# Optimization experiments

Measured on AMD Instinct MI355X. Metric: run time of the kernel, lower is better.

Reference implementation:

```python
import jax, jax.numpy as jnp
import numpy as np

C = 36   # num_classes
H = 256  # hidden_dim


def setup_inputs() -> dict:
    key = jax.random.key(0)
    ks = jax.random.split(key, 12)
    B, L, Dl, Dg = 32, 196, 1024, 1024
    s = lambda d: 1.0 / np.sqrt(d)
    return {
        "local_features": jax.random.normal(ks[0], (B, L, Dl), jnp.float32),
        "global_average_pool": jax.random.normal(ks[1], (B, Dg), jnp.float32),
        "Wl": jax.random.normal(ks[2], (Dl, C * H), jnp.float32) * s(Dl),
        "bl": jax.random.normal(ks[3], (C * H,), jnp.float32) * s(Dl),
        "Wg": jax.random.normal(ks[4], (Dg, C * H), jnp.float32) * s(Dg),
        "bg": jax.random.normal(ks[5], (C * H,), jnp.float32) * s(Dg),
        "Wh": jax.random.normal(ks[6], (H, H), jnp.float32) * s(H),
        "bh": jax.random.normal(ks[7], (H,), jnp.float32) * s(H),
        "Wr": jax.random.normal(ks[8], (H, 4), jnp.float32) * s(H),
        "br": jax.random.normal(ks[9], (4,), jnp.float32) * s(H),
        "Wc": jax.random.normal(ks[10], (H, 1), jnp.float32) * s(H),
        "bc": jax.random.normal(ks[11], (1,), jnp.float32) * s(H),
    }


def reference(local_features, global_average_pool, Wl, bl, Wg, bg, Wh, bh, Wr, br, Wc, bc):
    B, L, _ = local_features.shape
    # global projection -> [B, C, H]
    xg = (global_average_pool @ Wg + bg).reshape(B, C, H)
    # local projection -> [B, L, C, H] -> [B, C, L, H]
    xl = (local_features @ Wl + bl).reshape(B, L, C, H).transpose(0, 2, 1, 3)
    # per-class attention scores over locations: [B, C, L]
    dot = jnp.einsum('bch,bclh->bcl', xg, xl)
    attn = jax.nn.softmax(dot, axis=-1)
    # attention-weighted sum over locations: [B, C, H]
    ws = jnp.einsum('bcl,bclh->bch', attn, xl)
    hid = jax.nn.relu(ws @ Wh + bh)
    bbox_coords = (hid @ Wr + br).reshape(B, C * 4)   # [B, 4C]
    bbox_presence = (hid @ Wc + bc)[..., 0]           # [B, C]
    return bbox_coords, bbox_presence
```

## Files before the change

kernel.cpp:

```cpp
#include <hip/hip_runtime.h>
#include <stdint.h>

#define NCLS 36
#define HDIM 256
#define BSZ  32
#define LLOC 196
#define DIN  1024
#define NCH  9216
#define NCH4 2304
#define XG_N 294912
#define SC_N 225792
#define SC_N4 56448
#define V_N  1179648

__device__ __forceinline__ void fma4(float4& a, float s, const float4& b) {
  a.x += s * b.x; a.y += s * b.y; a.z += s * b.z; a.w += s * b.w;
}
__device__ __forceinline__ float dot4(const float4& a, const float4& b) {
  return a.x * b.x + a.y * b.y + a.z * b.z + a.w * b.w;
}

__global__ __launch_bounds__(256) void kA_xg(
    const float* __restrict__ Wg, const float* __restrict__ gap,
    float* __restrict__ XGP) {
  __shared__ __align__(16) float4 gs[1024];
  const int tid = threadIdx.x;
  const int nt = blockIdx.x, ks = blockIdx.y;
  const int n0 = nt * 128, k0 = ks * 128;
  const float4* gap4 = (const float4*)gap;
  for (int i = tid; i < 1024; i += 256)
    gs[i] = gap4[(size_t)(i >> 5) * 256 + ks * 32 + (i & 31)];
  __syncthreads();
  const int ng = tid & 31, b0 = (tid >> 5) * 4;
  float4 acc[4] = {};
  const float* wp = Wg + (size_t)k0 * NCH + n0 + ng * 4;
  #pragma unroll 4
  for (int k4 = 0; k4 < 32; ++k4) {
    float4 w[4];
    #pragma unroll
    for (int kk = 0; kk < 4; ++kk)
      w[kk] = *(const float4*)(wp + (size_t)(k4 * 4 + kk) * NCH);
    #pragma unroll
    for (int bb = 0; bb < 4; ++bb) {
      float4 g = gs[(b0 + bb) * 32 + k4];
      fma4(acc[bb], g.x, w[0]); fma4(acc[bb], g.y, w[1]);
      fma4(acc[bb], g.z, w[2]); fma4(acc[bb], g.w, w[3]);
    }
  }
  #pragma unroll
  for (int bb = 0; bb < 4; ++bb)
    *(float4*)&XGP[(size_t)ks * XG_N + (size_t)(b0 + bb) * NCH + n0 + ng * 4] = acc[bb];
}

__global__ __launch_bounds__(256) void kB_red(
    const float* __restrict__ XGP, const float* __restrict__ bg,
    float* __restrict__ XG) {
  const int b = blockIdx.x / 9;
  const int j = (blockIdx.x % 9) * 256 + threadIdx.x;
  const size_t off = (size_t)b * NCH4 + j;
  const float4* p4 = (const float4*)XGP;
  float4 s = ((const float4*)bg)[j];
  #pragma unroll
  for (int p = 0; p < 8; ++p) {
    float4 t = p4[(size_t)p * (XG_N / 4) + off];
    s.x += t.x; s.y += t.y; s.z += t.z; s.w += t.w;
  }
  ((float4*)XG)[off] = s;
}

__global__ __launch_bounds__(128) void kC_V(
    const float* __restrict__ Wl, const float* __restrict__ XG,
    float* __restrict__ V) {
  __shared__ __align__(16) float4 xs[2048];
  const int tid = threadIdx.x;
  const int c = blockIdx.x, kt = blockIdx.y;
  const int k0 = kt * 32;
  const float4* xg4 = (const float4*)XG;
  for (int i = tid; i < 2048; i += 128) {
    int b = i >> 6, h4 = i & 63;
    xs[i] = xg4[(size_t)b * NCH4 + c * 64 + h4];
  }
  __syncthreads();
  const int lane = tid & 63, wv_ = tid >> 6;
  const int q = lane & 3, r = lane >> 2;
  const int b0 = wv_ * 16;
  const int krow = k0 + r * 2;
  float acc0[16] = {}; float acc1[16] = {};
  const float* wl = Wl + (size_t)krow * NCH + c * 256 + q * 4;
  #pragma unroll 4
  for (int it = 0; it < 16; ++it) {
    float4 w0 = *(const float4*)(wl + it * 16);
    float4 w1 = *(const float4*)(wl + NCH + it * 16);
    #pragma unroll
    for (int bb = 0; bb < 16; ++bb) {
      float4 x = xs[(b0 + bb) * 64 + it * 4 + q];
      acc0[bb] += dot4(w0, x);
      acc1[bb] += dot4(w1, x);
    }
  }
  #pragma unroll
  for (int bb = 0; bb < 16; ++bb) {
    float s0 = acc0[bb], s1 = acc1[bb];
    s0 += __shfl_xor(s0, 1); s0 += __shfl_xor(s0, 2);
    s1 += __shfl_xor(s1, 1); s1 += __shfl_xor(s1, 2);
    acc0[bb] = s0; acc1[bb] = s1;
  }
  if (q == 0) {
    #pragma unroll
    for (int bb = 0; bb < 16; ++bb) {
      size_t o = (size_t)((b0 + bb) * NCLS + c) * DIN + krow;
      V[o]     = acc0[bb];
      V[o + 1] = acc1[bb];
    }
  }
}

__global__ __launch_bounds__(256) void kD_scores(
    const float* __restrict__ local_f, const float* __restrict__ V,
    float* __restrict__ SCP) {
  __shared__ __align__(16) float4 loc_s[3136];
  __shared__ __align__(16) float4 v_s[576];
  const int tid = threadIdx.x;
  const int b = blockIdx.x, ks = blockIdx.y;
  const float4* lf4 = (const float4*)local_f;
  for (int i = tid; i < 3136; i += 256) {
    int r = i >> 4, g = i & 15;
    loc_s[r * 16 + ((g + r) & 15)] = lf4[(size_t)(b * LLOC + r) * 256 + ks * 16 + g];
  }
  const float4* v4 = (const float4*)V;
  for (int i = tid; i < 576; i += 256) {
    int cc = i >> 4, g = i & 15;
    v_s[i] = v4[(size_t)(b * NCLS + cc) * 256 + ks * 16 + g];
  }
  __syncthreads();
  const int lg = tid & 63, cg = tid >> 6;
  float acc[4][9] = {};
  for (int k4 = 0; k4 < 16; ++k4) {
    float4 vv[9];
    #pragma unroll
    for (int ci = 0; ci < 9; ++ci) vv[ci] = v_s[(cg * 9 + ci) * 16 + k4];
    #pragma unroll
    for (int i = 0; i < 4; ++i) {
      int l = lg + 64 * i;
      if (l < LLOC) {
        float4 a = loc_s[l * 16 + ((k4 + l) & 15)];
        #pragma unroll
        for (int ci = 0; ci < 9; ++ci) acc[i][ci] += dot4(a, vv[ci]);
      }
    }
  }
  #pragma unroll
  for (int i = 0; i < 4; ++i) {
    int l = lg + 64 * i;
    if (l < LLOC) {
      #pragma unroll
      for (int ci = 0; ci < 9; ++ci)
        SCP[(size_t)ks * SC_N + (size_t)(b * NCLS + cg * 9 + ci) * LLOC + l] = acc[i][ci];
    }
  }
}

__global__ __launch_bounds__(64) void kE_softmax(
    const float* __restrict__ SCP, float* __restrict__ ATT) {
  const int b = blockIdx.x, c = blockIdx.y, t = threadIdx.x;
  const size_t base4 = (size_t)(b * NCLS + c) * 49;
  const float4* s4 = (const float4*)SCP;
  float4 s = {0.f, 0.f, 0.f, 0.f};
  float m = -1e30f;
  if (t < 49) {
    s = s4[base4 + t];
    #pragma unroll
    for (int p = 1; p < 16; ++p) {
      float4 x = s4[(size_t)p * SC_N4 + base4 + t];
      s.x += x.x; s.y += x.y; s.z += x.z; s.w += x.w;
    }
    m = fmaxf(fmaxf(s.x, s.y), fmaxf(s.z, s.w));
  }
  #pragma unroll
  for (int off = 32; off >= 1; off >>= 1) m = fmaxf(m, __shfl_xor(m, off));
  float4 e = {0.f, 0.f, 0.f, 0.f};
  float sum = 0.f;
  if (t < 49) {
    e.x = __expf(s.x - m); e.y = __expf(s.y - m);
    e.z = __expf(s.z - m); e.w = __expf(s.w - m);
    sum = e.x + e.y + e.z + e.w;
  }
  #pragma unroll
  for (int off = 32; off >= 1; off >>= 1) sum += __shfl_xor(sum, off);
  float inv = 1.0f / sum;
  if (t < 49) {
    e.x *= inv; e.y *= inv; e.z *= inv; e.w *= inv;
    ((float4*)ATT)[base4 + t] = e;
  }
}

__global__ __launch_bounds__(256) void kF_U(
    const float* __restrict__ local_f, const float* __restrict__ ATT,
    float* __restrict__ U) {
  __shared__ __align__(16) float4 att_s[1764];
  __shared__ __align__(16) float4 red[4608];
  const int tid = threadIdx.x;
  const int b = blockIdx.x, ks = blockIdx.y;
  const int k0 = ks * 128;
  const float4* at4 = (const float4*)ATT;
  for (int i = tid; i < 1764; i += 256) {
    int cc = i / 49, l4 = i - cc * 49;
    att_s[i] = at4[(size_t)(b * NCLS + cc) * 49 + l4];
  }
  __syncthreads();
  const int kg = tid & 15, cg = (tid >> 4) & 3, lh = tid >> 6;
  float4 acc[9][2] = {};
  const float* lbase = local_f + (size_t)b * LLOC * DIN + k0 + kg * 8;
  for (int l4 = lh; l4 < 49; l4 += 4) {
    float4 lv[4][2];
    #pragma unroll
    for (int ll = 0; ll < 4; ++ll) {
      const float* p = lbase + (size_t)(l4 * 4 + ll) * DIN;
      lv[ll][0] = *(const float4*)p;
      lv[ll][1] = *(const float4*)(p + 4);
    }
    #pragma unroll
    for (int ci = 0; ci < 9; ++ci) {
      float4 av = att_s[(cg * 9 + ci) * 49 + l4];
      fma4(acc[ci][0], av.x, lv[0][0]); fma4(acc[ci][1], av.x, lv[0][1]);
      fma4(acc[ci][0], av.y, lv[1][0]); fma4(acc[ci][1], av.y, lv[1][1]);
      fma4(acc[ci][0], av.z, lv[2][0]); fma4(acc[ci][1], av.z, lv[2][1]);
      fma4(acc[ci][0], av.w, lv[3][0]); fma4(acc[ci][1], av.w, lv[3][1]);
    }
  }
  #pragma unroll
  for (int ci = 0; ci < 9; ++ci) {
    int c = cg * 9 + ci;
    red[lh * 1152 + c * 32 + kg * 2 + 0] = acc[ci][0];
    red[lh * 1152 + c * 32 + kg * 2 + 1] = acc[ci][1];
  }
  __syncthreads();
  float4* u4 = (float4*)U;
  for (int i = tid; i < 1152; i += 256) {
    float4 s = red[i];
    #pragma unroll
    for (int p = 1; p < 4; ++p) {
      float4 t = red[p * 1152 + i];
      s.x += t.x; s.y += t.y; s.z += t.z; s.w += t.w;
    }
    u4[(size_t)(b * NCLS + (i >> 5)) * 256 + ks * 32 + (i & 31)] = s;
  }
}

__global__ __launch_bounds__(256) void kG_ws(
    const float* __restrict__ Wl, const float* __restrict__ U,
    float* __restrict__ WSP) {
  __shared__ __align__(16) float4 us[1024];
  const int tid = threadIdx.x;
  const int nt = blockIdx.x, ks = blockIdx.y;
  const int c = nt >> 1, h0 = (nt & 1) * 128, k0 = ks * 128;
  const float4* u4 = (const float4*)U;
  for (int i = tid; i < 1024; i += 256)
    us[i] = u4[(size_t)((i >> 5) * NCLS + c) * 256 + ks * 32 + (i & 31)];
  __syncthreads();
  const int ng = tid & 31, b0 = (tid >> 5) * 4;
  float4 acc[4] = {};
  const float* wp = Wl + (size_t)k0 * NCH + c * HDIM + h0 + ng * 4;
  #pragma unroll 4
  for (int k4 = 0; k4 < 32; ++k4) {
    float4 w[4];
    #pragma unroll
    for (int kk = 0; kk < 4; ++kk)
      w[kk] = *(const float4*)(wp + (size_t)(k4 * 4 + kk) * NCH);
    #pragma unroll
    for (int bb = 0; bb < 4; ++bb) {
      float4 g = us[(b0 + bb) * 32 + k4];
      fma4(acc[bb], g.x, w[0]); fma4(acc[bb], g.y, w[1]);
      fma4(acc[bb], g.z, w[2]); fma4(acc[bb], g.w, w[3]);
    }
  }
  #pragma unroll
  for (int bb = 0; bb < 4; ++bb)
    *(float4*)&WSP[(size_t)ks * XG_N + (size_t)(b0 + bb) * NCH + c * HDIM + h0 + ng * 4]
        = acc[bb];
}

__global__ __launch_bounds__(256) void kH_heads(
    const float* __restrict__ Wh, const float* __restrict__ bh,
    const float* __restrict__ Wr, const float* __restrict__ br,
    const float* __restrict__ Wc, const float* __restrict__ bc,
    const float* __restrict__ bl,
    const float* __restrict__ WSP, float* __restrict__ out) {
  __shared__ float ws_s[3][HDIM];
  __shared__ float hid_s[3][HDIM];
  const int b = blockIdx.x, c0 = blockIdx.y * 3;
  const int j = threadIdx.x;
  #pragma unroll
  for (int ci = 0; ci < 3; ++ci) {
    size_t base = (size_t)b * NCH + (c0 + ci) * HDIM + j;
    float s = bl[(c0 + ci) * HDIM + j];
    #pragma unroll
    for (int p = 0; p < 8; ++p) s += WSP[(size_t)p * XG_N + base];
    ws_s[ci][j] = s;
  }
  __syncthreads();
  float acc[3] = {0, 0, 0};
  for (int h = 0; h < HDIM; ++h) {
    float whj = Wh[(size_t)h * HDIM + j];
    acc[0] += ws_s[0][h] * whj;
    acc[1] += ws_s[1][h] * whj;
    acc[2] += ws_s[2][h] * whj;
  }
  float bj = bh[j];
  #pragma unroll
  for (int ci = 0; ci < 3; ++ci) hid_s[ci][j] = fmaxf(acc[ci] + bj, 0.0f);
  __syncthreads();
  const int r = j >> 6, j0 = j & 63;
  for (int ci = 0; ci < 3; ++ci) {
    const int c = c0 + ci;
    float s = 0.f;
    #pragma unroll
    for (int m = 0; m < 4; ++m)
      s += hid_s[ci][j0 + 64 * m] * Wr[(j0 + 64 * m) * 4 + r];
    #pragma unroll
    for (int off = 32; off >= 1; off >>= 1) s += __shfl_xor(s, off);
    if (j0 == 0) out[(size_t)b * (NCLS * 4) + c * 4 + r] = s + br[r];
    if (r == 0) {
      float p = 0.f;
      #pragma unroll
      for (int m = 0; m < 4; ++m)
        p += hid_s[ci][j0 + 64 * m] * Wc[j0 + 64 * m];
      #pragma unroll
      for (int off = 32; off >= 1; off >>= 1) p += __shfl_xor(p, off);
      if (j0 == 0) out[BSZ * NCLS * 4 + b * NCLS + c] = p + bc[0];
    }
  }
}

extern "C" void kernel_launch(void* const* d_in, const int* in_sizes, int n_in,
                              void* d_out, int out_size, void* d_ws, size_t ws_size,
                              hipStream_t stream) {
  const float* local = (const float*)d_in[0];
  const float* gap   = (const float*)d_in[1];
  const float* Wl    = (const float*)d_in[2];
  const float* bl    = (const float*)d_in[3];
  const float* Wg    = (const float*)d_in[4];
  const float* bg    = (const float*)d_in[5];
  const float* Wh    = (const float*)d_in[6];
  const float* bh    = (const float*)d_in[7];
  const float* Wr    = (const float*)d_in[8];
  const float* br    = (const float*)d_in[9];
  const float* Wc    = (const float*)d_in[10];
  const float* bc    = (const float*)d_in[11];
  float* out         = (float*)d_out;

  float* XGP = (float*)d_ws;
  float* XG  = XGP + (size_t)8 * XG_N;
  float* V   = XG + XG_N;
  float* SCP = V + V_N;
  float* ATT = SCP + (size_t)16 * SC_N;
  float* U   = ATT + SC_N;
  float* WSP = U + V_N;

  kA_xg     <<<dim3(72, 8),  dim3(256), 0, stream>>>(Wg, gap, XGP);
  kB_red    <<<dim3(288),    dim3(256), 0, stream>>>(XGP, bg, XG);
  kC_V      <<<dim3(36, 32), dim3(128), 0, stream>>>(Wl, XG, V);
  kD_scores <<<dim3(32, 16), dim3(256), 0, stream>>>(local, V, SCP);
  kE_softmax<<<dim3(32, 36), dim3(64),  0, stream>>>(SCP, ATT);
  kF_U      <<<dim3(32, 8),  dim3(256), 0, stream>>>(local, ATT, U);
  kG_ws     <<<dim3(72, 8),  dim3(256), 0, stream>>>(Wl, U, WSP);
  kH_heads  <<<dim3(32, 12), dim3(256), 0, stream>>>(Wh, bh, Wr, br, Wc, bc, bl, WSP, out);
}
```

Measured before the change: 288.3 us.

## Retile weight GEMMs so each weight is loaded once per block

The two skinny GEMM kernels (global projection and weighted-sum projection) are restructured. Each thread now holds accumulators for all 32 batch rows of a 4-column slice, and the four waves split a 64-deep K chunk between them, with the wave partials combined through shared memory. Previously several thread groups in a block re-read the same weight rows; now each weight element is fetched once per block, cutting redundant global/cache traffic on the weight streams. In exchange, the split-K factor doubles from 8 to 16, so the downstream reduction kernels read twice as many partials and more workspace is written. The kernels also use heavy register pressure (128 accumulator floats) and about 72KB of LDS, which limits occupancy.

```diff
diff --git a/kernel.cpp b/kernel.cpp
--- a/kernel.cpp
+++ b/kernel.cpp
@@ -23,33 +23,55 @@
 __global__ __launch_bounds__(256) void kA_xg(
     const float* __restrict__ Wg, const float* __restrict__ gap,
     float* __restrict__ XGP) {
-  __shared__ __align__(16) float4 gs[1024];
+  __shared__ __align__(16) float4 gs[512];
+  __shared__ __align__(16) float4 red[4096];
   const int tid = threadIdx.x;
   const int nt = blockIdx.x, ks = blockIdx.y;
-  const int n0 = nt * 128, k0 = ks * 128;
+  const int n0 = nt * 256, k0 = ks * 64;
   const float4* gap4 = (const float4*)gap;
-  for (int i = tid; i < 1024; i += 256)
-    gs[i] = gap4[(size_t)(i >> 5) * 256 + ks * 32 + (i & 31)];
-  __syncthreads();
-  const int ng = tid & 31, b0 = (tid >> 5) * 4;
-  float4 acc[4] = {};
-  const float* wp = Wg + (size_t)k0 * NCH + n0 + ng * 4;
-  #pragma unroll 4
-  for (int k4 = 0; k4 < 32; ++k4) {
-    float4 w[4];
+  for (int i = tid; i < 512; i += 256)
+    gs[i] = gap4[(size_t)(i >> 4) * 256 + ks * 16 + (i & 15)];
+  __syncthreads();
+  const int w = tid >> 6, lane = tid & 63;
+  float4 acc[32] = {};
+  const float* wp = Wg + (size_t)(k0 + w * 16) * NCH + n0 + lane * 4;
+  for (int kq = 0; kq < 4; ++kq) {
+    float4 wr[4];
     #pragma unroll
     for (int kk = 0; kk < 4; ++kk)
-      w[kk] = *(const float4*)(wp + (size_t)(k4 * 4 + kk) * NCH);
-    #pragma unroll
-    for (int bb = 0; bb < 4; ++bb) {
-      float4 g = gs[(b0 + bb) * 32 + k4];
-      fma4(acc[bb], g.x, w[0]); fma4(acc[bb], g.y, w[1]);
-      fma4(acc[bb], g.z, w[2]); fma4(acc[bb], g.w, w[3]);
-    }
-  }
-  #pragma unroll
-  for (int bb = 0; bb < 4; ++bb)
-    *(float4*)&XGP[(size_t)ks * XG_N + (size_t)(b0 + bb) * NCH + n0 + ng * 4] = acc[bb];
+      wr[kk] = *(const float4*)(wp + (size_t)(kq * 4 + kk) * NCH);
+    const int k4g = w * 4 + kq;
+    #pragma unroll
+    for (int b = 0; b < 32; ++b) {
+      float4 g = gs[b * 16 + k4g];
+      fma4(acc[b], g.x, wr[0]); fma4(acc[b], g.y, wr[1]);
+      fma4(acc[b], g.z, wr[2]); fma4(acc[b], g.w, wr[3]);
+    }
+  }
+  __syncthreads();
+  if (w >= 2) {
+    #pragma unroll
+    for (int b = 0; b < 32; ++b) red[(w - 2) * 2048 + b * 64 + lane] = acc[b];
+  }
+  __syncthreads();
+  if (w < 2) {
+    #pragma unroll
+    for (int b = 0; b < 32; ++b) {
+      float4 t = red[w * 2048 + b * 64 + lane];
+      acc[b].x += t.x; acc[b].y += t.y; acc[b].z += t.z; acc[b].w += t.w;
+    }
+    #pragma unroll
+    for (int b = 0; b < 32; ++b) red[w * 2048 + b * 64 + lane] = acc[b];
+  }
+  __syncthreads();
+  #pragma unroll
+  for (int i = 0; i < 8; ++i) {
+    int b = w * 8 + i;
+    float4 a = red[b * 64 + lane];
+    float4 c = red[2048 + b * 64 + lane];
+    a.x += c.x; a.y += c.y; a.z += c.z; a.w += c.w;
+    *(float4*)&XGP[(size_t)ks * XG_N + (size_t)b * NCH + n0 + lane * 4] = a;
+  }
 }
 
 __global__ __launch_bounds__(256) void kB_red(
@@ -61,7 +83,7 @@
   const float4* p4 = (const float4*)XGP;
   float4 s = ((const float4*)bg)[j];
   #pragma unroll
-  for (int p = 0; p < 8; ++p) {
+  for (int p = 0; p < 16; ++p) {
     float4 t = p4[(size_t)p * (XG_N / 4) + off];
     s.x += t.x; s.y += t.y; s.z += t.z; s.w += t.w;
   }
@@ -250,34 +272,55 @@
 __global__ __launch_bounds__(256) void kG_ws(
     const float* __restrict__ Wl, const float* __restrict__ U,
     float* __restrict__ WSP) {
-  __shared__ __align__(16) float4 us[1024];
+  __shared__ __align__(16) float4 us[512];
+  __shared__ __align__(16) float4 red[4096];
   const int tid = threadIdx.x;
-  const int nt = blockIdx.x, ks = blockIdx.y;
-  const int c = nt >> 1, h0 = (nt & 1) * 128, k0 = ks * 128;
+  const int c = blockIdx.x, ks = blockIdx.y;
+  const int k0 = ks * 64;
   const float4* u4 = (const float4*)U;
-  for (int i = tid; i < 1024; i += 256)
-    us[i] = u4[(size_t)((i >> 5) * NCLS + c) * 256 + ks * 32 + (i & 31)];
-  __syncthreads();
-  const int ng = tid & 31, b0 = (tid >> 5) * 4;
-  float4 acc[4] = {};
-  const float* wp = Wl + (size_t)k0 * NCH + c * HDIM + h0 + ng * 4;
-  #pragma unroll 4
-  for (int k4 = 0; k4 < 32; ++k4) {
-    float4 w[4];
+  for (int i = tid; i < 512; i += 256)
+    us[i] = u4[(size_t)((i >> 4) * NCLS + c) * 256 + ks * 16 + (i & 15)];
+  __syncthreads();
+  const int w = tid >> 6, lane = tid & 63;
+  float4 acc[32] = {};
+  const float* wp = Wl + (size_t)(k0 + w * 16) * NCH + c * HDIM + lane * 4;
+  for (int kq = 0; kq < 4; ++kq) {
+    float4 wr[4];
     #pragma unroll
     for (int kk = 0; kk < 4; ++kk)
-      w[kk] = *(const float4*)(wp + (size_t)(k4 * 4 + kk) * NCH);
-    #pragma unroll
-    for (int bb = 0; bb < 4; ++bb) {
-      float4 g = us[(b0 + bb) * 32 + k4];
-      fma4(acc[bb], g.x, w[0]); fma4(acc[bb], g.y, w[1]);
-      fma4(acc[bb], g.z, w[2]); fma4(acc[bb], g.w, w[3]);
-    }
-  }
-  #pragma unroll
-  for (int bb = 0; bb < 4; ++bb)
-    *(float4*)&WSP[(size_t)ks * XG_N + (size_t)(b0 + bb) * NCH + c * HDIM + h0 + ng * 4]
-        = acc[bb];
+      wr[kk] = *(const float4*)(wp + (size_t)(kq * 4 + kk) * NCH);
+    const int k4g = w * 4 + kq;
+    #pragma unroll
+    for (int b = 0; b < 32; ++b) {
+      float4 g = us[b * 16 + k4g];
+      fma4(acc[b], g.x, wr[0]); fma4(acc[b], g.y, wr[1]);
+      fma4(acc[b], g.z, wr[2]); fma4(acc[b], g.w, wr[3]);
+    }
+  }
+  __syncthreads();
+  if (w >= 2) {
+    #pragma unroll
+    for (int b = 0; b < 32; ++b) red[(w - 2) * 2048 + b * 64 + lane] = acc[b];
+  }
+  __syncthreads();
+  if (w < 2) {
+    #pragma unroll
+    for (int b = 0; b < 32; ++b) {
+      float4 t = red[w * 2048 + b * 64 + lane];
+      acc[b].x += t.x; acc[b].y += t.y; acc[b].z += t.z; acc[b].w += t.w;
+    }
+    #pragma unroll
+    for (int b = 0; b < 32; ++b) red[w * 2048 + b * 64 + lane] = acc[b];
+  }
+  __syncthreads();
+  #pragma unroll
+  for (int i = 0; i < 8; ++i) {
+    int b = w * 8 + i;
+    float4 a = red[b * 64 + lane];
+    float4 cc = red[2048 + b * 64 + lane];
+    a.x += cc.x; a.y += cc.y; a.z += cc.z; a.w += cc.w;
+    *(float4*)&WSP[(size_t)ks * XG_N + (size_t)b * NCH + c * HDIM + lane * 4] = a;
+  }
 }
 
 __global__ __launch_bounds__(256) void kH_heads(
@@ -295,7 +338,7 @@
     size_t base = (size_t)b * NCH + (c0 + ci) * HDIM + j;
     float s = bl[(c0 + ci) * HDIM + j];
     #pragma unroll
-    for (int p = 0; p < 8; ++p) s += WSP[(size_t)p * XG_N + base];
+    for (int p = 0; p < 16; ++p) s += WSP[(size_t)p * XG_N + base];
     ws_s[ci][j] = s;
   }
   __syncthreads();
@@ -350,19 +393,19 @@
   float* out         = (float*)d_out;
 
   float* XGP = (float*)d_ws;
-  float* XG  = XGP + (size_t)8 * XG_N;
+  float* XG  = XGP + (size_t)16 * XG_N;
   float* V   = XG + XG_N;
   float* SCP = V + V_N;
   float* ATT = SCP + (size_t)16 * SC_N;
   float* U   = ATT + SC_N;
   float* WSP = U + V_N;
 
-  kA_xg     <<<dim3(72, 8),  dim3(256), 0, stream>>>(Wg, gap, XGP);
+  kA_xg     <<<dim3(36, 16), dim3(256), 0, stream>>>(Wg, gap, XGP);
   kB_red    <<<dim3(288),    dim3(256), 0, stream>>>(XGP, bg, XG);
   kC_V      <<<dim3(36, 32), dim3(128), 0, stream>>>(Wl, XG, V);
   kD_scores <<<dim3(32, 16), dim3(256), 0, stream>>>(local, V, SCP);
   kE_softmax<<<dim3(32, 36), dim3(64),  0, stream>>>(SCP, ATT);
   kF_U      <<<dim3(32, 8),  dim3(256), 0, stream>>>(local, ATT, U);
-  kG_ws     <<<dim3(72, 8),  dim3(256), 0, stream>>>(Wl, U, WSP);
+  kG_ws     <<<dim3(36, 16), dim3(256), 0, stream>>>(Wl, U, WSP);
   kH_heads  <<<dim3(32, 12), dim3(256), 0, stream>>>(Wh, bh, Wr, br, Wc, bc, bl, WSP, out);
 }
```

Result: faster. 267.9 us (-7.1%).
